# Performance work log

Hardware: AMD Instinct MI355X
Metric: run time of the kernel (lower is better)

The kernel has to match this reference:

```python
import jax, jax.numpy as jnp
import numpy as np

IN_C, OUT_C, K, N_FILTERS, STRIDE, PAD = 256, 512, 3, 64, 1, 1


def setup_inputs() -> dict:
    key = jax.random.key(0)
    kx, kw, kb, krw, krb = jax.random.split(key, 5)
    fan_in = IN_C * K * K
    bound = 1.0 / np.sqrt(fan_in)
    x = jax.random.normal(kx, (32, IN_C, 56, 56), dtype=jnp.float32)
    weight = jax.random.uniform(kw, (OUT_C, IN_C, K, K), minval=-bound, maxval=bound, dtype=jnp.float32)
    bias = jax.random.uniform(kb, (OUT_C,), minval=-bound, maxval=bound, dtype=jnp.float32)
    rbound = 1.0 / np.sqrt(IN_C)
    router_w = jax.random.uniform(krw, (OUT_C, IN_C), minval=-rbound, maxval=rbound, dtype=jnp.float32)
    router_b = jax.random.uniform(krb, (OUT_C,), minval=-rbound, maxval=rbound, dtype=jnp.float32)
    return {"x": x, "weight": weight, "bias": bias, "router_w": router_w, "router_b": router_b}


def reference(x, weight, bias, router_w, router_b):
    B = x.shape[0]
    # router: global avg pool -> linear -> top-k channel mask
    pooled = jnp.mean(x, axis=(2, 3))                      # [B, IN_C]
    router_out = pooled @ router_w.T + router_b            # [B, OUT_C]
    _, top_idx = jax.lax.top_k(router_out, N_FILTERS)      # [B, k]
    mask = jnp.zeros((B, OUT_C), dtype=x.dtype).at[jnp.arange(B)[:, None], top_idx].set(1.0)
    # dense conv2d
    conv = jax.lax.conv_general_dilated(
        x, weight, window_strides=(STRIDE, STRIDE), padding=[(PAD, PAD), (PAD, PAD)],
        dimension_numbers=("NCHW", "OIHW", "NCHW"))
    conv = conv + bias[None, :, None, None]
    return conv * mask[:, :, None, None]
```

## Files before the change

kernel.cpp:

```cpp
#include <hip/hip_runtime.h>

#define IN_C   256
#define OUT_C  512
#define WIDTH  56
#define HW     3136
#define KTOT   2304
#define NF     64
#define NU     448
#define NB     32
#define NGRP   8
#define TN     64
#define NTILE  49
#define SROWS  192

typedef __bf16 bf16x8 __attribute__((ext_vector_type(8)));
typedef float  f32x4  __attribute__((ext_vector_type(4)));

__global__ __launch_bounds__(256) void xpose_kernel(const float* __restrict__ x,
                                                    __bf16* __restrict__ xT,
                                                    float* __restrict__ partial) {
    int id = blockIdx.x;
    int b = id / NTILE, tile = id - b * NTILE;
    int ptile = tile * TN;
    int tid = threadIdx.x;
    __shared__ float tl[64][65];
    __shared__ float plsum[IN_C];
    const float* xb  = x + (size_t)b * IN_C * HW + ptile;
    __bf16*      xtb = xT + ((size_t)b * HW + ptile) * IN_C;
    int pxq  = tid & 15;
    int rowi = tid >> 4;
    int px   = tid >> 2;
    int icq  = tid & 3;
    for (int chunk = 0; chunk < 4; ++chunk) {
        #pragma unroll
        for (int r = 0; r < 4; ++r) {
            int icL = r * 16 + rowi;
            int ic  = chunk * 64 + icL;
            float4 v = *(const float4*)(xb + (size_t)ic * HW + pxq * 4);
            *(float4*)&tl[icL][pxq * 4] = v;
            float s = v.x + v.y + v.z + v.w;
            s += __shfl_down(s, 8, 16);
            s += __shfl_down(s, 4, 16);
            s += __shfl_down(s, 2, 16);
            s += __shfl_down(s, 1, 16);
            if (pxq == 0) plsum[ic] = s;
        }
        __syncthreads();
        bf16x8 o0, o1;
        #pragma unroll
        for (int k = 0; k < 8; ++k) o0[k] = (__bf16)tl[icq * 16 + k][px];
        #pragma unroll
        for (int k = 0; k < 8; ++k) o1[k] = (__bf16)tl[icq * 16 + 8 + k][px];
        __bf16* dst = xtb + (size_t)px * IN_C + chunk * 64 + icq * 16;
        *(bf16x8*)dst = o0;
        *(bf16x8*)(dst + 8) = o1;
        __syncthreads();
    }
    partial[(size_t)id * IN_C + tid] = plsum[tid];
}

__global__ __launch_bounds__(256) void wfrag_kernel(const float* __restrict__ w,
                                                    __bf16* __restrict__ wf) {
    int oc = blockIdx.x;
    const float* src = w + (size_t)oc * KTOT;
    __bf16* dst = wf + (size_t)oc * KTOT;
    int tid = threadIdx.x;
    #pragma unroll
    for (int rr = 0; rr < 9; ++rr) {
        int i = rr * 256 + tid;
        float v = src[i];
        int ic = i / 9, tap = i - ic * 9;
        dst[((ic >> 5) * 9 + tap) * 32 + (ic & 31)] = (__bf16)v;
    }
}

__global__ __launch_bounds__(512) void router_kernel(const float* __restrict__ partial,
                                                     const float* __restrict__ rw,
                                                     const float* __restrict__ rb,
                                                     int* __restrict__ sel,
                                                     int* __restrict__ unsel) {
    int b = blockIdx.x;
    __shared__ float p[IN_C];
    __shared__ float v[OUT_C];
    __shared__ int   scount, ucount;
    int t = threadIdx.x;
    if (t < IN_C) {
        float s = 0.f;
        const float* pb = partial + (size_t)b * NTILE * IN_C + t;
        for (int k = 0; k < NTILE; ++k) s += pb[k * IN_C];
        p[t] = s * (1.0f / HW);
    }
    if (t == 0) { scount = 0; ucount = 0; }
    __syncthreads();
    float acc = rb[t];
    const float* wrow = rw + (size_t)t * IN_C;
    for (int i = 0; i < IN_C; ++i) acc += p[i] * wrow[i];
    v[t] = acc;
    __syncthreads();
    int cnt = 0;
    for (int j = 0; j < OUT_C; ++j) {
        float o = v[j];
        cnt += (o > acc) || (o == acc && j < t);
    }
    if (cnt < NF) {
        int pos = atomicAdd(&scount, 1);
        sel[b * NF + pos] = t;
    } else {
        int pos = atomicAdd(&ucount, 1);
        unsel[b * NU + pos] = t;
    }
}

__global__ __launch_bounds__(256, 4) void conv_kernel(const __bf16* __restrict__ xT,
                                                      const __bf16* __restrict__ wf,
                                                      const float* __restrict__ bias,
                                                      const int* __restrict__ sel,
                                                      const int* __restrict__ unsel,
                                                      float* __restrict__ out) {
    int id   = blockIdx.x;
    int xcd  = id & 7, slot = id >> 3;
    int bq   = slot / NTILE;
    int tile = slot - bq * NTILE;
    int b    = xcd * 4 + bq;
    int ptile = tile * TN;

    int tid  = threadIdx.x;
    int lane = tid & 63, w = tid >> 6;
    int fm   = lane & 15, fq = lane >> 4;
    int mi2  = w >> 1,  s2 = w & 1;

    __shared__ __bf16 xlds[2][SROWS * 32];
    __shared__ int    selLds[NF];
    __shared__ int    unsLds[NU];

    size_t outb = (size_t)b * OUT_C * HW;
    const __bf16* xtb = xT + (size_t)b * HW * IN_C;

    if (tid < NF) selLds[tid] = sel[b * NF + tid];
    for (int u = tid; u < NU; u += 256) unsLds[u] = unsel[b * NU + u];

    const __bf16* sga[3];
    #pragma unroll
    for (int rnd = 0; rnd < 3; ++rnd) {
        int row = rnd * 64 + w * 16 + (lane >> 2);
        int cc  = (lane & 3) ^ ((row >> 1) & 3);
        int gp  = ptile - 57 + row;
        gp = gp < 0 ? 0 : (gp > HW - 1 ? HW - 1 : gp);
        sga[rnd] = xtb + (size_t)gp * IN_C + cc * 8;
    }

#define STAGE(buf, g) { \
    _Pragma("unroll") \
    for (int rnd = 0; rnd < 3; ++rnd) \
        __builtin_amdgcn_global_load_lds( \
            (const __attribute__((address_space(1))) void*)(sga[rnd] + (g) * 32), \
            (__attribute__((address_space(3))) void*)&xlds[buf][(rnd * 64 + w * 16) * 32], \
            16, 0, 0); }

    int pp[2], poh[2], pow_[2];
    #pragma unroll
    for (int sl = 0; sl < 2; ++sl) {
        int p = ptile + (s2 * 2 + sl) * 16 + fm;
        pp[sl]   = p;
        poh[sl]  = p / WIDTH;
        pow_[sl] = p - poh[sl] * WIDTH;
    }

    f32x4 acc[2][2] = {};

    STAGE(0, 0);
    __syncthreads();

    {
        f32x4 z = {0.f, 0.f, 0.f, 0.f};
        int lq = tid & 15;
        for (int u = tid >> 4; u < NU; u += 16) {
            int oc = unsLds[u];
            __builtin_nontemporal_store(z, (f32x4*)(out + outb + (size_t)oc * HW + ptile) + lq);
        }
    }

    const __bf16* pA[2];
    #pragma unroll
    for (int m = 0; m < 2; ++m)
        pA[m] = wf + (size_t)selLds[(mi2 * 2 + m) * 16 + fm] * KTOT;

    #pragma unroll 1
    for (int g = 0; g < NGRP; ++g) {
        int cur = g & 1;
        if (g < NGRP - 1) STAGE(cur ^ 1, g + 1);
        const int gof = g * 9 * 32;
        #pragma unroll
        for (int t9 = 0; t9 < 9; ++t9) {
            const int r = t9 / 3, c = t9 - 3 * r;
            const int shift = (r - 1) * WIDTH + (c - 1);
            bf16x8 af0 = *(const bf16x8*)(pA[0] + gof + t9 * 32 + fq * 8);
            bf16x8 af1 = *(const bf16x8*)(pA[1] + gof + t9 * 32 + fq * 8);
            #pragma unroll
            for (int sl = 0; sl < 2; ++sl) {
                int row = (s2 * 2 + sl) * 16 + fm + 57 + shift;
                int ohr = poh[sl] + r - 1, owc = pow_[sl] + c - 1;
                bool ok = ((unsigned)ohr < 56u) && ((unsigned)owc < 56u);
                int sw = fq ^ ((row >> 1) & 3);
                bf16x8 bfr = *(const bf16x8*)&xlds[cur][row * 32 + sw * 8];
                bf16x8 zz = {};
                bfr = ok ? bfr : zz;
                acc[0][sl] = __builtin_amdgcn_mfma_f32_16x16x32_bf16(af0, bfr, acc[0][sl], 0, 0, 0);
                acc[1][sl] = __builtin_amdgcn_mfma_f32_16x16x32_bf16(af1, bfr, acc[1][sl], 0, 0, 0);
            }
        }
        __syncthreads();
    }

    #pragma unroll
    for (int m = 0; m < 2; ++m) {
        int mi = mi2 * 2 + m;
        #pragma unroll
        for (int reg = 0; reg < 4; ++reg) {
            int oc = selLds[mi * 16 + fq * 4 + reg];
            float bs = bias[oc];
            float* orow = out + outb + (size_t)oc * HW;
            #pragma unroll
            for (int sl = 0; sl < 2; ++sl)
                __builtin_nontemporal_store(acc[m][sl][reg] + bs, &orow[pp[sl]]);
        }
    }
#undef STAGE
}

extern "C" void kernel_launch(void* const* d_in, const int* in_sizes, int n_in,
                              void* d_out, int out_size, void* d_ws, size_t ws_size,
                              hipStream_t stream) {
    (void)in_sizes; (void)n_in; (void)ws_size; (void)out_size;
    const float* x        = (const float*)d_in[0];
    const float* weight   = (const float*)d_in[1];
    const float* bias     = (const float*)d_in[2];
    const float* router_w = (const float*)d_in[3];
    const float* router_b = (const float*)d_in[4];
    float* out = (float*)d_out;

    char* ws = (char*)d_ws;
    float*  partial = (float*)ws;
    int*    sel     = (int*)(ws + 0x200000);
    int*    unsel   = (int*)(ws + 0x202000);
    __bf16* wfb     = (__bf16*)(ws + 0x220000);
    __bf16* xT      = (__bf16*)(ws + 0x480000);

    xpose_kernel <<<NB * NTILE, 256, 0, stream>>>(x, xT, partial);
    wfrag_kernel <<<OUT_C,      256, 0, stream>>>(weight, wfb);
    router_kernel<<<NB,         512, 0, stream>>>(partial, router_w, router_b, sel, unsel);
    conv_kernel  <<<NTILE * NB, 256, 0, stream>>>(xT, wfb, bias, sel, unsel, out);
}
```

Baseline: 440.0 us.

## Precompact selected weights per batch into MFMA fragment layout and prefetch per group

Adds an acomp kernel that gathers each batch's 64 selected filters into a contiguous, fragment-ordered A buffer, so the conv kernel reads coalesced weight fragments instead of scattered rows. The conv kernel now preloads all 18 A fragments for a channel group before issuing the next LDS stage, and it zero-fills unselected channels straight from global before staging. The weight reorder kernel goes through shared memory to write vectorized bf16x8 stores, and the router matvec becomes wave-parallel with shuffle reductions. In exchange there is an extra kernel launch and ~9MB of workspace, and register pressure rises, with launch bounds relaxed to 2 blocks per SM.

```diff
diff --git a/kernel.cpp b/kernel.cpp
--- a/kernel.cpp
+++ b/kernel.cpp
@@ -62,15 +62,23 @@
 __global__ __launch_bounds__(256) void wfrag_kernel(const float* __restrict__ w,
                                                     __bf16* __restrict__ wf) {
     int oc = blockIdx.x;
+    __shared__ float sm[KTOT];
     const float* src = w + (size_t)oc * KTOT;
+    int tid = threadIdx.x;
+    #pragma unroll
+    for (int k = 0; k < 9; ++k) sm[k * 256 + tid] = src[k * 256 + tid];
+    __syncthreads();
     __bf16* dst = wf + (size_t)oc * KTOT;
-    int tid = threadIdx.x;
-    #pragma unroll
-    for (int rr = 0; rr < 9; ++rr) {
-        int i = rr * 256 + tid;
-        float v = src[i];
-        int ic = i / 9, tap = i - ic * 9;
-        dst[((ic >> 5) * 9 + tap) * 32 + (ic & 31)] = (__bf16)v;
+    for (int C = tid; C < 288; C += 256) {
+        int d0  = C * 8;
+        int icg = d0 / 288;
+        int rem = d0 - icg * 288;
+        int tap = rem >> 5, icl0 = rem & 31;
+        bf16x8 o;
+        #pragma unroll
+        for (int j = 0; j < 8; ++j)
+            o[j] = (__bf16)sm[(icg * 32 + icl0 + j) * 9 + tap];
+        *(bf16x8*)&dst[d0] = o;
     }
 }
 
@@ -92,11 +100,18 @@
     }
     if (t == 0) { scount = 0; ucount = 0; }
     __syncthreads();
-    float acc = rb[t];
-    const float* wrow = rw + (size_t)t * IN_C;
-    for (int i = 0; i < IN_C; ++i) acc += p[i] * wrow[i];
-    v[t] = acc;
-    __syncthreads();
+    int w = t >> 6, lane = t & 63;
+    float4 pl = *(const float4*)&p[lane * 4];
+    for (int k = 0; k < 64; ++k) {
+        int oc = w * 64 + k;
+        float4 wv = *(const float4*)&rw[(size_t)oc * IN_C + lane * 4];
+        float d = pl.x * wv.x + pl.y * wv.y + pl.z * wv.z + pl.w * wv.w;
+        #pragma unroll
+        for (int off = 32; off > 0; off >>= 1) d += __shfl_down(d, off, 64);
+        if (lane == 0) v[oc] = d + rb[oc];
+    }
+    __syncthreads();
+    float acc = v[t];
     int cnt = 0;
     for (int j = 0; j < OUT_C; ++j) {
         float o = v[j];
@@ -111,8 +126,27 @@
     }
 }
 
-__global__ __launch_bounds__(256, 4) void conv_kernel(const __bf16* __restrict__ xT,
-                                                      const __bf16* __restrict__ wf,
+__global__ __launch_bounds__(256) void acomp_kernel(const __bf16* __restrict__ wf,
+                                                    const int* __restrict__ sel,
+                                                    __bf16* __restrict__ A) {
+    int blk = blockIdx.x;
+    int b = blk >> 3, part = blk & 7;
+    __shared__ int s[NF];
+    int tid = threadIdx.x;
+    if (tid < NF) s[tid] = sel[b * NF + tid];
+    __syncthreads();
+    __bf16* dst = A + (size_t)b * (NF * KTOT);
+    #pragma unroll
+    for (int c = part * 9; c < part * 9 + 9; ++c) {
+        int C = c * 256 + tid;
+        int icl8 = C & 3, oc = (C >> 2) & 63, gt = C >> 8;
+        bf16x8 vv = *(const bf16x8*)&wf[(size_t)s[oc] * KTOT + gt * 32 + icl8 * 8];
+        *(bf16x8*)&dst[(size_t)C * 8] = vv;
+    }
+}
+
+__global__ __launch_bounds__(256, 2) void conv_kernel(const __bf16* __restrict__ xT,
+                                                      const __bf16* __restrict__ Ac,
                                                       const float* __restrict__ bias,
                                                       const int* __restrict__ sel,
                                                       const int* __restrict__ unsel,
@@ -131,13 +165,22 @@
 
     __shared__ __bf16 xlds[2][SROWS * 32];
     __shared__ int    selLds[NF];
-    __shared__ int    unsLds[NU];
 
     size_t outb = (size_t)b * OUT_C * HW;
     const __bf16* xtb = xT + (size_t)b * HW * IN_C;
+    const __bf16* ab  = Ac + (size_t)b * (NF * KTOT);
 
     if (tid < NF) selLds[tid] = sel[b * NF + tid];
-    for (int u = tid; u < NU; u += 256) unsLds[u] = unsel[b * NU + u];
+
+    {
+        const int* ub = unsel + b * NU;
+        f32x4 z = {0.f, 0.f, 0.f, 0.f};
+        int lq = tid & 15;
+        for (int u = tid >> 4; u < NU; u += 16) {
+            int oc = ub[u];
+            __builtin_nontemporal_store(z, (f32x4*)(out + outb + (size_t)oc * HW + ptile) + lq);
+        }
+    }
 
     const __bf16* sga[3];
     #pragma unroll
@@ -171,31 +214,23 @@
     STAGE(0, 0);
     __syncthreads();
 
-    {
-        f32x4 z = {0.f, 0.f, 0.f, 0.f};
-        int lq = tid & 15;
-        for (int u = tid >> 4; u < NU; u += 16) {
-            int oc = unsLds[u];
-            __builtin_nontemporal_store(z, (f32x4*)(out + outb + (size_t)oc * HW + ptile) + lq);
-        }
-    }
-
-    const __bf16* pA[2];
-    #pragma unroll
-    for (int m = 0; m < 2; ++m)
-        pA[m] = wf + (size_t)selLds[(mi2 * 2 + m) * 16 + fm] * KTOT;
-
     #pragma unroll 1
     for (int g = 0; g < NGRP; ++g) {
         int cur = g & 1;
+        bf16x8 af[2][9];
+        const __bf16* agp = ab + (size_t)(g * 9) * 2048;
+        #pragma unroll
+        for (int t9 = 0; t9 < 9; ++t9) {
+            #pragma unroll
+            for (int m = 0; m < 2; ++m)
+                af[m][t9] = *(const bf16x8*)(agp + (size_t)t9 * 2048
+                                             + ((mi2 * 2 + m) * 16 + fm) * 32 + fq * 8);
+        }
         if (g < NGRP - 1) STAGE(cur ^ 1, g + 1);
-        const int gof = g * 9 * 32;
         #pragma unroll
         for (int t9 = 0; t9 < 9; ++t9) {
             const int r = t9 / 3, c = t9 - 3 * r;
             const int shift = (r - 1) * WIDTH + (c - 1);
-            bf16x8 af0 = *(const bf16x8*)(pA[0] + gof + t9 * 32 + fq * 8);
-            bf16x8 af1 = *(const bf16x8*)(pA[1] + gof + t9 * 32 + fq * 8);
             #pragma unroll
             for (int sl = 0; sl < 2; ++sl) {
                 int row = (s2 * 2 + sl) * 16 + fm + 57 + shift;
@@ -205,8 +240,8 @@
                 bf16x8 bfr = *(const bf16x8*)&xlds[cur][row * 32 + sw * 8];
                 bf16x8 zz = {};
                 bfr = ok ? bfr : zz;
-                acc[0][sl] = __builtin_amdgcn_mfma_f32_16x16x32_bf16(af0, bfr, acc[0][sl], 0, 0, 0);
-                acc[1][sl] = __builtin_amdgcn_mfma_f32_16x16x32_bf16(af1, bfr, acc[1][sl], 0, 0, 0);
+                acc[0][sl] = __builtin_amdgcn_mfma_f32_16x16x32_bf16(af[0][t9], bfr, acc[0][sl], 0, 0, 0);
+                acc[1][sl] = __builtin_amdgcn_mfma_f32_16x16x32_bf16(af[1][t9], bfr, acc[1][sl], 0, 0, 0);
             }
         }
         __syncthreads();
@@ -240,14 +275,16 @@
     float* out = (float*)d_out;
 
     char* ws = (char*)d_ws;
+    __bf16* Acomp   = (__bf16*)ws;
     float*  partial = (float*)ws;
-    int*    sel     = (int*)(ws + 0x200000);
-    int*    unsel   = (int*)(ws + 0x202000);
-    __bf16* wfb     = (__bf16*)(ws + 0x220000);
-    __bf16* xT      = (__bf16*)(ws + 0x480000);
+    __bf16* wfb     = (__bf16*)(ws + 0x900000);
+    int*    sel     = (int*)(ws + 0xB40000);
+    int*    unsel   = (int*)(ws + 0xB42000);
+    __bf16* xT      = (__bf16*)(ws + 0xB50000);
 
     xpose_kernel <<<NB * NTILE, 256, 0, stream>>>(x, xT, partial);
     wfrag_kernel <<<OUT_C,      256, 0, stream>>>(weight, wfb);
     router_kernel<<<NB,         512, 0, stream>>>(partial, router_w, router_b, sel, unsel);
-    conv_kernel  <<<NTILE * NB, 256, 0, stream>>>(xT, wfb, bias, sel, unsel, out);
-}
+    acomp_kernel <<<NB * 8,     256, 0, stream>>>(wfb, sel, Acomp);
+    conv_kernel  <<<NTILE * NB, 256, 0, stream>>>(xT, Acomp, bias, sel, unsel, out);
+}
```

Result: faster. 430.7 us (-2.1%).
